# Performance work log

Hardware: AMD Instinct MI355X
Metric: run time of the kernel (lower is better)

## Reference

```python
import jax, jax.numpy as jnp
import numpy as np

THRE = 4.0  # ReLUX threshold / multispike lens
EPS = 1e-5  # BatchNorm eps (torch default)

@jax.custom_vjp
def spike(x):
    # multispike forward: floor(clamp(x,0,4)+0.5)
    return jnp.floor(jnp.clip(x, 0.0, THRE) + 0.5)

def _spike_fwd(x):
    return spike(x), x

def _spike_bwd(x, g):
    # surrogate gradient: pass-through on 0 < x < lens
    return (g * ((x > 0) & (x < THRE)).astype(g.dtype),)

spike.defvjp(_spike_fwd, _spike_bwd)


def setup_inputs() -> dict:
    key = jax.random.key(0)
    k0, k1, k2 = jax.random.split(key, 3)
    B, N, C = 4, 1024, 512
    x = jax.random.normal(k0, (B, N, C), jnp.float32)
    Wqkv = jax.random.normal(k1, (3 * C, C), jnp.float32) * (C ** -0.5)  # Linear weight [out,in], no bias
    gamma = jnp.ones((3 * C,), jnp.float32)   # BN weight
    beta = jnp.zeros((3 * C,), jnp.float32)   # BN bias
    Wproj = jax.random.normal(k2, (C, C), jnp.float32) * (C ** -0.5)
    bproj = jnp.zeros((C,), jnp.float32)
    return {"x": x, "Wqkv": Wqkv, "gamma": gamma, "beta": beta, "Wproj": Wproj, "bproj": bproj}


def reference(x, Wqkv, gamma, beta, Wproj, bproj):
    B, N, C = x.shape
    H = 8
    hd = C // H
    scale = hd ** -0.5

    xs = spike(x)                                    # head_spike
    qkv = jnp.einsum('bnc,dc->bnd', xs, Wqkv)        # [B,N,3C]
    # BatchNorm1d over channel dim with batch stats across (B, N)
    mu = qkv.mean(axis=(0, 1))
    var = qkv.var(axis=(0, 1))
    qkv = (qkv - mu) * jax.lax.rsqrt(var + EPS) * gamma + beta

    qkv = qkv.reshape(B, N, 3, H, hd).transpose(2, 0, 3, 1, 4)  # [3,B,H,N,hd]
    q = spike(qkv[0])
    k = spike(qkv[1])
    v = spike(qkv[2])

    attn = jnp.einsum('bhnd,bhmd->bhnm', q, k)       # no softmax
    attn = spike(attn)
    out = jnp.einsum('bhnm,bhmd->bhnd', attn, v) * scale
    out = out.transpose(0, 2, 1, 3).reshape(B, N, C)
    out = spike(out)                                 # project_spike
    return jnp.einsum('bnc,dc->bnd', out, Wproj) + bproj
```

## Files before the change

kernel.cpp:

```cpp
#include <hip/hip_runtime.h>

typedef __attribute__((ext_vector_type(8))) short short8;
typedef __attribute__((ext_vector_type(4))) short short4v;
typedef __attribute__((ext_vector_type(8))) signed char s8x8;
typedef __attribute__((ext_vector_type(4))) unsigned char u8x4;
typedef __attribute__((ext_vector_type(4))) float f32x4;
typedef __attribute__((ext_vector_type(4))) int int4v;
typedef __attribute__((ext_vector_type(4))) unsigned int u32x4;

#define THRE 4.0f

#define GLOAD_LDS16(g, l) \
    __builtin_amdgcn_global_load_lds((const __attribute__((address_space(1))) void*)(g), \
                                     (__attribute__((address_space(3))) void*)(l), 16, 0, 0)

__device__ __forceinline__ float spikef(float x) {
    return floorf(fminf(fmaxf(x, 0.0f), THRE) + 0.5f);
}
__device__ __forceinline__ unsigned short f2bf(float f) {
    return (unsigned short)(__builtin_bit_cast(unsigned int, f) >> 16);
}
__device__ __forceinline__ unsigned short f2bf_rn(float f) {
    unsigned u = __builtin_bit_cast(unsigned int, f);
    unsigned r = ((u >> 16) & 1u) + 0x7FFFu;
    return (unsigned short)((u + r) >> 16);
}
__device__ __forceinline__ float bf2f(unsigned short s) {
    return __builtin_bit_cast(float, (unsigned int)s << 16);
}
__device__ __forceinline__ int4v mfma_i8(u32x4 a, u32x4 b, int4v c) {
    return __builtin_amdgcn_mfma_i32_16x16x64_i8(__builtin_bit_cast(int4v, a),
                                                 __builtin_bit_cast(int4v, b), c, 0, 0, 0);
}

__global__ void k_prep(const float* __restrict__ x,
                       const float* __restrict__ Wq, const float* __restrict__ Wp,
                       unsigned char* __restrict__ xs8, signed char* __restrict__ Wq8,
                       float* __restrict__ wscale, short* __restrict__ Wpd) {
    const int blk = blockIdx.x, tid = threadIdx.x;
    if (blk < 2048) {
        const int i = blk * 256 + tid;
        const float4 v = *(const float4*)&x[(size_t)i * 4];
        u8x4 o;
        o.x = (unsigned char)spikef(v.x);
        o.y = (unsigned char)spikef(v.y);
        o.z = (unsigned char)spikef(v.z);
        o.w = (unsigned char)spikef(v.w);
        *(u8x4*)&xs8[(size_t)i * 4] = o;
    } else if (blk < 2432) {
        const int row = (blk - 2048) * 4 + (tid >> 6);
        const int lane = tid & 63;
        const float* wr = Wq + (size_t)row * 512 + lane * 8;
        float w[8];
        float mx = 0.f;
        #pragma unroll
        for (int i = 0; i < 8; ++i) { w[i] = wr[i]; mx = fmaxf(mx, fabsf(w[i])); }
        #pragma unroll
        for (int o = 32; o > 0; o >>= 1) mx = fmaxf(mx, __shfl_xor(mx, o, 64));
        const float inv = mx > 0.f ? 127.0f / mx : 0.f;
        s8x8 q;
        #pragma unroll
        for (int i = 0; i < 8; ++i) q[i] = (signed char)rintf(w[i] * inv);
        *(s8x8*)&Wq8[(size_t)row * 512 + lane * 8] = q;
        if (lane == 0) wscale[row] = mx > 0.f ? mx / 127.0f : 0.f;
    } else {
        const int i = (blk - 2432) * 256 + tid;
        const float4 v = *(const float4*)&Wp[(size_t)i * 4];
        short4v o;
        o.x = (short)f2bf_rn(v.x);
        o.y = (short)f2bf_rn(v.y);
        o.z = (short)f2bf_rn(v.z);
        o.w = (short)f2bf_rn(v.w);
        *(short4v*)&Wpd[(size_t)i * 4] = o;
    }
}

__global__ __launch_bounds__(256) void k_gemm_qkv(const unsigned char* __restrict__ A,
                                                  const signed char* __restrict__ B,
                                                  const float* __restrict__ wscale,
                                                  short* __restrict__ C,
                                                  float* __restrict__ psum,
                                                  float* __restrict__ psq) {
    __shared__ __align__(16) unsigned char As[128 * 128];
    __shared__ __align__(16) unsigned char Bs[96 * 128];
    const int tid  = threadIdx.x;
    const int lane = tid & 63, wv = tid >> 6;
    const int wy = wv >> 1, wx = wv & 1;
    const int quad = lane >> 4, l16 = lane & 15;
    const int u = blockIdx.x;
    const int mtile = u & 31;
    const int m0 = mtile * 128, n0 = (u >> 5) * 96;
    const int N = 1536;

    int4v acc[4][3];
    #pragma unroll
    for (int i = 0; i < 4; ++i)
        #pragma unroll
        for (int j = 0; j < 3; ++j)
            #pragma unroll
            for (int r = 0; r < 4; ++r) acc[i][j][r] = 0;

    const unsigned char* gA[4]; unsigned char* lA[4];
    #pragma unroll
    for (int i = 0; i < 4; ++i) {
        int L = wv + 4 * i;
        int c = L * 64 + lane;
        int r = c >> 3, g = (c & 7) ^ (r & 7);
        gA[i] = A + (size_t)(m0 + r) * 512 + g * 16;
        lA[i] = &As[(size_t)c * 16];
    }
    const unsigned char* gB[3]; unsigned char* lB[3];
    #pragma unroll
    for (int i = 0; i < 3; ++i) {
        int L = wv + 4 * i;
        int c = L * 64 + lane;
        int r = c >> 3, g = (c & 7) ^ (r & 7);
        gB[i] = (const unsigned char*)B + (size_t)(n0 + r) * 512 + g * 16;
        lB[i] = &Bs[(size_t)c * 16];
    }

    for (int k0 = 0; k0 < 512; k0 += 128) {
        __syncthreads();
        #pragma unroll
        for (int i = 0; i < 4; ++i) GLOAD_LDS16(gA[i] + k0, lA[i]);
        #pragma unroll
        for (int i = 0; i < 3; ++i) GLOAD_LDS16(gB[i] + k0, lB[i]);
        __syncthreads();
        #pragma unroll
        for (int kk = 0; kk < 2; ++kk) {
            u32x4 aF[4], bF[3];
            #pragma unroll
            for (int mt = 0; mt < 4; ++mt) {
                const int r = wy * 64 + mt * 16 + l16;
                aF[mt] = *(const u32x4*)&As[(size_t)r * 128 + (((kk * 4 + quad) ^ (r & 7)) * 16)];
            }
            #pragma unroll
            for (int nt = 0; nt < 3; ++nt) {
                const int r = wx * 48 + nt * 16 + l16;
                bF[nt] = *(const u32x4*)&Bs[(size_t)r * 128 + (((kk * 4 + quad) ^ (r & 7)) * 16)];
            }
            #pragma unroll
            for (int mt = 0; mt < 4; ++mt)
                #pragma unroll
                for (int nt = 0; nt < 3; ++nt)
                    acc[mt][nt] = mfma_i8(aF[mt], bF[nt], acc[mt][nt]);
        }
    }

    float sc[3];
    #pragma unroll
    for (int nt = 0; nt < 3; ++nt) sc[nt] = wscale[n0 + wx * 48 + nt * 16 + l16];

    float vacc[4][3][4];
    #pragma unroll
    for (int mt = 0; mt < 4; ++mt)
        #pragma unroll
        for (int r = 0; r < 4; ++r) {
            int row = m0 + wy * 64 + mt * 16 + quad * 4 + r;
            short* Cr = C + (size_t)row * N + n0 + wx * 48 + l16;
            #pragma unroll
            for (int nt = 0; nt < 3; ++nt) {
                float v = (float)acc[mt][nt][r] * sc[nt];
                vacc[mt][nt][r] = v;
                Cr[nt * 16] = (short)f2bf_rn(v);
            }
        }

    __syncthreads();
    float* PS = (float*)As;
    float* PQ = (float*)Bs;
    #pragma unroll
    for (int nt = 0; nt < 3; ++nt) {
        float s = 0.f, q = 0.f;
        #pragma unroll
        for (int mt = 0; mt < 4; ++mt)
            #pragma unroll
            for (int r = 0; r < 4; ++r) {
                float v = vacc[mt][nt][r];
                s += v;
                q = fmaf(v, v, q);
            }
        PS[(wy * 4 + quad) * 96 + wx * 48 + nt * 16 + l16] = s;
        PQ[(wy * 4 + quad) * 96 + wx * 48 + nt * 16 + l16] = q;
    }
    __syncthreads();
    if (tid < 96) {
        float s = 0.f, q = 0.f;
        #pragma unroll
        for (int i = 0; i < 8; ++i) { s += PS[i * 96 + tid]; q += PQ[i * 96 + tid]; }
        psum[mtile * 1536 + n0 + tid] = s;
        psq [mtile * 1536 + n0 + tid] = q;
    }
}

__global__ __launch_bounds__(256) void k_gemm_proj(const short* __restrict__ A,
                                                   const short* __restrict__ B,
                                                   const float* __restrict__ bias,
                                                   float* __restrict__ C) {
    __shared__ __align__(16) short As[32 * 64];
    __shared__ __align__(16) short Bs[128 * 64];
    const int tid  = threadIdx.x;
    const int lane = tid & 63, wv = tid >> 6;
    const int wy = wv >> 1, wx = wv & 1;
    const int quad = lane >> 4, l16 = lane & 15;
    const int u = blockIdx.x;
    const int mtile = u & 127;
    const int m0 = mtile * 32, n0 = (u >> 7) * 128;
    const int K = 512, N = 512;

    f32x4 acc[4];
    #pragma unroll
    for (int j = 0; j < 4; ++j)
        #pragma unroll
        for (int r = 0; r < 4; ++r) acc[j][r] = 0.f;

    const short* gA0; short* lA0;
    {
        int c = tid;
        int r = c >> 3, g = (c & 7) ^ (r & 7);
        gA0 = A + (size_t)(m0 + r) * K + g * 8;
        lA0 = &As[(size_t)c * 8];
    }
    const short* gB[4]; short* lB[4];
    #pragma unroll
    for (int i = 0; i < 4; ++i) {
        int c = tid + 256 * i;
        int r = c >> 3, g = (c & 7) ^ (r & 7);
        gB[i] = B + (size_t)(n0 + r) * K + g * 8;
        lB[i] = &Bs[(size_t)c * 8];
    }

    for (int k0 = 0; k0 < K; k0 += 64) {
        __syncthreads();
        GLOAD_LDS16(gA0 + k0, lA0);
        #pragma unroll
        for (int i = 0; i < 4; ++i) GLOAD_LDS16(gB[i] + k0, lB[i]);
        __syncthreads();
        #pragma unroll
        for (int kk = 0; kk < 2; ++kk) {
            const int ra = wy * 16 + l16;
            short8 aF = *(const short8*)&As[(size_t)ra * 64 + (((kk * 4 + quad) ^ (ra & 7)) * 8)];
            #pragma unroll
            for (int nt = 0; nt < 4; ++nt) {
                const int rb = wx * 64 + nt * 16 + l16;
                short8 bF = *(const short8*)&Bs[(size_t)rb * 64 + (((kk * 4 + quad) ^ (rb & 7)) * 8)];
                acc[nt] = __builtin_amdgcn_mfma_f32_16x16x32_bf16(aF, bF, acc[nt], 0, 0, 0);
            }
        }
    }

    float bs[4];
    #pragma unroll
    for (int nt = 0; nt < 4; ++nt) bs[nt] = bias[n0 + wx * 64 + nt * 16 + l16];
    #pragma unroll
    for (int r = 0; r < 4; ++r) {
        int row = m0 + wy * 16 + quad * 4 + r;
        float* Cr = C + (size_t)row * N + n0 + wx * 64 + l16;
        #pragma unroll
        for (int nt = 0; nt < 4; ++nt) Cr[nt * 16] = acc[nt][r] + bs[nt];
    }
}

__global__ __launch_bounds__(256) void k_bn_spike(const short* __restrict__ qkvb,
                           const float* __restrict__ psum, const float* __restrict__ psq,
                           const float* __restrict__ gamma, const float* __restrict__ beta,
                           unsigned char* __restrict__ qp, unsigned char* __restrict__ kp,
                           unsigned char* __restrict__ vt) {
    __shared__ float sa[64], sb[64];
    __shared__ __align__(16) unsigned char tile[64 * 80];
    const int tid = threadIdx.x;
    const int slice = blockIdx.x;
    const int c0 = slice * 64;
    const int r0 = blockIdx.y * 256;
    const int b = r0 >> 10, nb = r0 & 1023;

    if (tid < 64) {
        const int c = c0 + tid;
        double s = 0.0, q = 0.0;
        for (int st = 0; st < 32; ++st) { s += (double)psum[st * 1536 + c]; q += (double)psq[st * 1536 + c]; }
        const double mu  = s / 4096.0;
        const double var = q / 4096.0 - mu * mu;
        const float a = (float)((double)gamma[c] / sqrt(var + 1e-5));
        sa[tid] = a;
        sb[tid] = fmaf(-(float)mu, a, beta[c]);
    }
    __syncthreads();

    if (slice < 16) {
        const int h = slice & 7;
        const int ch4 = (tid & 15) * 4, rr = tid >> 4;
        const float4 A4 = *(const float4*)&sa[ch4];
        const float4 B4 = *(const float4*)&sb[ch4];
        unsigned char* base = (slice < 8 ? qp : kp) + (((size_t)b * 8 + h) * 1024 + nb) * 64;
        for (int i = rr; i < 256; i += 16) {
            const short4v v4 = *(const short4v*)&qkvb[(size_t)(r0 + i) * 1536 + c0 + ch4];
            u8x4 o;
            o.x = (unsigned char)spikef(fmaf(bf2f((unsigned short)v4.x), A4.x, B4.x));
            o.y = (unsigned char)spikef(fmaf(bf2f((unsigned short)v4.y), A4.y, B4.y));
            o.z = (unsigned char)spikef(fmaf(bf2f((unsigned short)v4.z), A4.z, B4.z));
            o.w = (unsigned char)spikef(fmaf(bf2f((unsigned short)v4.w), A4.w, B4.w));
            *(u8x4*)&base[(size_t)i * 64 + ch4] = o;
        }
    } else {
        const int h = slice - 16;
        const int ch = tid & 63, rq = tid >> 6;
        const float A = sa[ch], Bsh = sb[ch];
        const int e = tid >> 2, j0 = (tid & 3) * 16;
        unsigned char* vbase = vt + (size_t)b * 524288 + (size_t)h * 65536
                             + (size_t)(nb >> 8) * 16384 + e * 64 + j0;
        for (int rb = 0; rb < 4; ++rb) {
            __syncthreads();
            for (int i = rq; i < 64; i += 4) {
                float v = bf2f((unsigned short)qkvb[(size_t)(r0 + rb * 64 + i) * 1536 + c0 + ch]);
                tile[ch * 80 + i] = (unsigned char)spikef(fmaf(v, A, Bsh));
            }
            __syncthreads();
            *(u32x4*)&vbase[rb * 4096] = *(const u32x4*)&tile[e * 80 + j0];
        }
    }
}

__global__ __launch_bounds__(256) void k_attn(const unsigned char* __restrict__ qp,
                                              const unsigned char* __restrict__ kp,
                                              const unsigned char* __restrict__ vt,
                                              short* __restrict__ sout) {
    __shared__ __align__(16) unsigned int Sb[2][64 * 68];
    const int tid  = threadIdx.x;
    const int lane = tid & 63, w = tid >> 6;
    const int quad = lane >> 4, l16 = lane & 15;
    const int u = blockIdx.x;
    const int bhid = u & 31;
    const int b = bhid >> 3, h = bhid & 7;
    const int n0 = (u >> 5) * 64;
    const size_t bh = (size_t)b * 8 + h;

    const unsigned char* Kb = kp + bh * 65536;
    const unsigned char* Vb = vt + bh * 65536;

    u32x4 qf[4];
    #pragma unroll
    for (int mt = 0; mt < 4; ++mt)
        qf[mt] = *(const u32x4*)&qp[(bh * 1024 + n0 + mt * 16 + l16) * 64 + quad * 16];

    int4v of[4];
    #pragma unroll
    for (int mt = 0; mt < 4; ++mt)
        #pragma unroll
        for (int r = 0; r < 4; ++r) of[mt][r] = 0;

    u32x4 kfc[4];
    #pragma unroll
    for (int jt = 0; jt < 4; ++jt)
        kfc[jt] = *(const u32x4*)&Kb[(size_t)(w * 64 + jt * 16 + l16) * 64 + quad * 16];

    #pragma unroll
    for (int t = 0; t < 4; ++t) {
        u32x4 bV[4];
        #pragma unroll
        for (int kk = 0; kk < 4; ++kk)
            bV[kk] = *(const u32x4*)&Vb[(size_t)((t * 4 + kk) * 64 + w * 16 + l16) * 64 + quad * 16];

        __builtin_amdgcn_s_setprio(1);
        #pragma unroll
        for (int jt = 0; jt < 4; ++jt) {
            #pragma unroll
            for (int mt = 0; mt < 4; ++mt) {
                int4v z;
                #pragma unroll
                for (int r = 0; r < 4; ++r) z[r] = 0;
                int4v s = mfma_i8(kfc[jt], qf[mt], z);
                unsigned int pkk = 0;
                #pragma unroll
                for (int r = 0; r < 4; ++r) {
                    int v = s[r]; v = v < 0 ? 0 : (v > 4 ? 4 : v);
                    pkk |= (unsigned int)v << (8 * r);
                }
                Sb[t & 1][(mt * 16 + l16) * 68 + w * 16 + jt * 4 + quad] = pkk;
            }
        }
        __builtin_amdgcn_s_setprio(0);
        __syncthreads();

        if (t < 3) {
            #pragma unroll
            for (int jt = 0; jt < 4; ++jt)
                kfc[jt] = *(const u32x4*)&Kb[(size_t)((t + 1) * 256 + w * 64 + jt * 16 + l16) * 64 + quad * 16];
        }

        __builtin_amdgcn_s_setprio(1);
        #pragma unroll
        for (int kk = 0; kk < 4; ++kk) {
            #pragma unroll
            for (int mt = 0; mt < 4; ++mt) {
                u32x4 aS = *(const u32x4*)&Sb[t & 1][(mt * 16 + l16) * 68 + kk * 16 + quad * 4];
                of[mt] = mfma_i8(aS, bV[kk], of[mt]);
            }
        }
        __builtin_amdgcn_s_setprio(0);
    }

    #pragma unroll
    for (int mt = 0; mt < 4; ++mt)
        #pragma unroll
        for (int r = 0; r < 4; ++r) {
            size_t orow = (size_t)b * 1024 + n0 + mt * 16 + quad * 4 + r;
            sout[orow * 512 + h * 64 + w * 16 + l16] =
                (short)f2bf(spikef((float)of[mt][r] * 0.125f));
        }
}

extern "C" void kernel_launch(void* const* d_in, const int* in_sizes, int n_in,
                              void* d_out, int out_size, void* d_ws, size_t ws_size,
                              hipStream_t stream) {
    const float* x     = (const float*)d_in[0];
    const float* Wqkv  = (const float*)d_in[1];
    const float* gamma = (const float*)d_in[2];
    const float* beta  = (const float*)d_in[3];
    const float* Wproj = (const float*)d_in[4];
    const float* bproj = (const float*)d_in[5];
    float* out = (float*)d_out;

    char* w = (char*)d_ws;
    unsigned char* xs8   = (unsigned char*)(w);
    signed char* Wq8     = (signed char*)(w + 8388608);
    float* wscale        = (float*)(w + 9437184);
    short* Wproj2        = (short*)(w + 11534336);
    short* qkvb          = (short*)(w + 12582912);
    unsigned char* qp    = (unsigned char*)(w + 37748736);
    unsigned char* kp    = (unsigned char*)(w + 41943040);
    unsigned char* vt    = (unsigned char*)(w + 46137344);
    float* psum          = (float*)(w + 50331648);
    float* psq           = psum + 32 * 1536;
    short* sout          = (short*)(w);

    k_prep<<<2688, 256, 0, stream>>>(x, Wqkv, Wproj, xs8, Wq8, wscale, Wproj2);
    k_gemm_qkv<<<512, 256, 0, stream>>>(xs8, Wq8, wscale, qkvb, psum, psq);
    k_bn_spike<<<dim3(24, 16), 256, 0, stream>>>(qkvb, psum, psq, gamma, beta, qp, kp, vt);
    k_attn<<<512, 256, 0, stream>>>(qp, kp, vt, sout);
    k_gemm_proj<<<512, 256, 0, stream>>>(sout, Wproj2, bproj, out);
}
```

Before: 108.9 us.

## Fuse input spike and weight int8 quantization into QKV GEMM, drop prep kernel

```diff
diff --git a/kernel.cpp b/kernel.cpp
--- a/kernel.cpp
+++ b/kernel.cpp
@@ -2,7 +2,6 @@
 
 typedef __attribute__((ext_vector_type(8))) short short8;
 typedef __attribute__((ext_vector_type(4))) short short4v;
-typedef __attribute__((ext_vector_type(8))) signed char s8x8;
 typedef __attribute__((ext_vector_type(4))) unsigned char u8x4;
 typedef __attribute__((ext_vector_type(4))) float f32x4;
 typedef __attribute__((ext_vector_type(4))) int int4v;
@@ -33,56 +32,14 @@
                                                  __builtin_bit_cast(int4v, b), c, 0, 0, 0);
 }
 
-__global__ void k_prep(const float* __restrict__ x,
-                       const float* __restrict__ Wq, const float* __restrict__ Wp,
-                       unsigned char* __restrict__ xs8, signed char* __restrict__ Wq8,
-                       float* __restrict__ wscale, short* __restrict__ Wpd) {
-    const int blk = blockIdx.x, tid = threadIdx.x;
-    if (blk < 2048) {
-        const int i = blk * 256 + tid;
-        const float4 v = *(const float4*)&x[(size_t)i * 4];
-        u8x4 o;
-        o.x = (unsigned char)spikef(v.x);
-        o.y = (unsigned char)spikef(v.y);
-        o.z = (unsigned char)spikef(v.z);
-        o.w = (unsigned char)spikef(v.w);
-        *(u8x4*)&xs8[(size_t)i * 4] = o;
-    } else if (blk < 2432) {
-        const int row = (blk - 2048) * 4 + (tid >> 6);
-        const int lane = tid & 63;
-        const float* wr = Wq + (size_t)row * 512 + lane * 8;
-        float w[8];
-        float mx = 0.f;
-        #pragma unroll
-        for (int i = 0; i < 8; ++i) { w[i] = wr[i]; mx = fmaxf(mx, fabsf(w[i])); }
-        #pragma unroll
-        for (int o = 32; o > 0; o >>= 1) mx = fmaxf(mx, __shfl_xor(mx, o, 64));
-        const float inv = mx > 0.f ? 127.0f / mx : 0.f;
-        s8x8 q;
-        #pragma unroll
-        for (int i = 0; i < 8; ++i) q[i] = (signed char)rintf(w[i] * inv);
-        *(s8x8*)&Wq8[(size_t)row * 512 + lane * 8] = q;
-        if (lane == 0) wscale[row] = mx > 0.f ? mx / 127.0f : 0.f;
-    } else {
-        const int i = (blk - 2432) * 256 + tid;
-        const float4 v = *(const float4*)&Wp[(size_t)i * 4];
-        short4v o;
-        o.x = (short)f2bf_rn(v.x);
-        o.y = (short)f2bf_rn(v.y);
-        o.z = (short)f2bf_rn(v.z);
-        o.w = (short)f2bf_rn(v.w);
-        *(short4v*)&Wpd[(size_t)i * 4] = o;
-    }
-}
-
-__global__ __launch_bounds__(256) void k_gemm_qkv(const unsigned char* __restrict__ A,
-                                                  const signed char* __restrict__ B,
-                                                  const float* __restrict__ wscale,
-                                                  short* __restrict__ C,
-                                                  float* __restrict__ psum,
-                                                  float* __restrict__ psq) {
+__global__ __launch_bounds__(256, 2) void k_qkv(const float* __restrict__ x,
+                                                const float* __restrict__ Wq,
+                                                short* __restrict__ C,
+                                                float* __restrict__ psum,
+                                                float* __restrict__ psq) {
     __shared__ __align__(16) unsigned char As[128 * 128];
-    __shared__ __align__(16) unsigned char Bs[96 * 128];
+    __shared__ __align__(16) unsigned char Bs[96 * 512];
+    __shared__ float invB[96], scB[96];
     const int tid  = threadIdx.x;
     const int lane = tid & 63, wv = tid >> 6;
     const int wy = wv >> 1, wx = wv & 1;
@@ -92,6 +49,56 @@
     const int m0 = mtile * 128, n0 = (u >> 5) * 96;
     const int N = 1536;
 
+    #pragma unroll
+    for (int rr = 0; rr < 3; ++rr) {
+        const int row = rr * 32 + (tid >> 3);
+        const int ln8 = tid & 7;
+        const float* wr = Wq + (size_t)(n0 + row) * 512 + ln8 * 64;
+        float mx = 0.f;
+        #pragma unroll
+        for (int i = 0; i < 16; ++i) {
+            const float4 f = *(const float4*)(wr + i * 4);
+            mx = fmaxf(mx, fmaxf(fmaxf(fabsf(f.x), fabsf(f.y)), fmaxf(fabsf(f.z), fabsf(f.w))));
+        }
+        mx = fmaxf(mx, __shfl_xor(mx, 1, 64));
+        mx = fmaxf(mx, __shfl_xor(mx, 2, 64));
+        mx = fmaxf(mx, __shfl_xor(mx, 4, 64));
+        if (ln8 == 0) {
+            invB[row] = mx > 0.f ? 127.0f / mx : 0.f;
+            scB[row]  = mx > 0.f ? mx / 127.0f : 0.f;
+        }
+    }
+    __syncthreads();
+
+    #pragma unroll
+    for (int i = 0; i < 12; ++i) {
+        const int idx = i * 256 + tid;
+        const int r = idx >> 5, ks = idx & 31;
+        const float* src = Wq + (size_t)(n0 + r) * 512 + ks * 16;
+        const float inv = invB[r];
+        u32x4 ov;
+        #pragma unroll
+        for (int d = 0; d < 4; ++d) {
+            const float4 f = *(const float4*)(src + d * 4);
+            unsigned dw  = ((unsigned)(int)rintf(f.x * inv)) & 255u;
+            dw |= (((unsigned)(int)rintf(f.y * inv)) & 255u) << 8;
+            dw |= (((unsigned)(int)rintf(f.z * inv)) & 255u) << 16;
+            dw |= (((unsigned)(int)rintf(f.w * inv)) & 255u) << 24;
+            ov[d] = dw;
+        }
+        *(u32x4*)&Bs[(size_t)r * 512 + (((ks & ~7) | ((ks & 7) ^ (r & 7))) * 16)] = ov;
+    }
+
+    float4 aPre[16];
+    #pragma unroll
+    for (int i = 0; i < 4; ++i) {
+        const int idx = i * 256 + tid;
+        const int r = idx >> 3, q = idx & 7;
+        const float* src = x + (size_t)(m0 + r) * 512 + q * 16;
+        #pragma unroll
+        for (int d = 0; d < 4; ++d) aPre[i * 4 + d] = *(const float4*)(src + d * 4);
+    }
+
     int4v acc[4][3];
     #pragma unroll
     for (int i = 0; i < 4; ++i)
@@ -100,32 +107,37 @@
             #pragma unroll
             for (int r = 0; r < 4; ++r) acc[i][j][r] = 0;
 
-    const unsigned char* gA[4]; unsigned char* lA[4];
-    #pragma unroll
-    for (int i = 0; i < 4; ++i) {
-        int L = wv + 4 * i;
-        int c = L * 64 + lane;
-        int r = c >> 3, g = (c & 7) ^ (r & 7);
-        gA[i] = A + (size_t)(m0 + r) * 512 + g * 16;
-        lA[i] = &As[(size_t)c * 16];
-    }
-    const unsigned char* gB[3]; unsigned char* lB[3];
-    #pragma unroll
-    for (int i = 0; i < 3; ++i) {
-        int L = wv + 4 * i;
-        int c = L * 64 + lane;
-        int r = c >> 3, g = (c & 7) ^ (r & 7);
-        gB[i] = (const unsigned char*)B + (size_t)(n0 + r) * 512 + g * 16;
-        lB[i] = &Bs[(size_t)c * 16];
-    }
-
-    for (int k0 = 0; k0 < 512; k0 += 128) {
+    for (int t = 0; t < 4; ++t) {
         __syncthreads();
         #pragma unroll
-        for (int i = 0; i < 4; ++i) GLOAD_LDS16(gA[i] + k0, lA[i]);
-        #pragma unroll
-        for (int i = 0; i < 3; ++i) GLOAD_LDS16(gB[i] + k0, lB[i]);
+        for (int i = 0; i < 4; ++i) {
+            const int idx = i * 256 + tid;
+            const int r = idx >> 3, q = idx & 7;
+            u32x4 ov;
+            #pragma unroll
+            for (int d = 0; d < 4; ++d) {
+                const float4 f = aPre[i * 4 + d];
+                unsigned dw  = (unsigned)(unsigned char)spikef(f.x);
+                dw |= (unsigned)(unsigned char)spikef(f.y) << 8;
+                dw |= (unsigned)(unsigned char)spikef(f.z) << 16;
+                dw |= (unsigned)(unsigned char)spikef(f.w) << 24;
+                ov[d] = dw;
+            }
+            *(u32x4*)&As[(size_t)r * 128 + ((q ^ (r & 7)) * 16)] = ov;
+        }
         __syncthreads();
+        if (t < 3) {
+            const int k0n = (t + 1) * 128;
+            #pragma unroll
+            for (int i = 0; i < 4; ++i) {
+                const int idx = i * 256 + tid;
+                const int r = idx >> 3, q = idx & 7;
+                const float* src = x + (size_t)(m0 + r) * 512 + k0n + q * 16;
+                #pragma unroll
+                for (int d = 0; d < 4; ++d) aPre[i * 4 + d] = *(const float4*)(src + d * 4);
+            }
+        }
+        const int k0 = t * 128;
         #pragma unroll
         for (int kk = 0; kk < 2; ++kk) {
             u32x4 aF[4], bF[3];
@@ -137,7 +149,7 @@
             #pragma unroll
             for (int nt = 0; nt < 3; ++nt) {
                 const int r = wx * 48 + nt * 16 + l16;
-                bF[nt] = *(const u32x4*)&Bs[(size_t)r * 128 + (((kk * 4 + quad) ^ (r & 7)) * 16)];
+                bF[nt] = *(const u32x4*)&Bs[(size_t)r * 512 + k0 + (((kk * 4 + quad) ^ (r & 7)) * 16)];
             }
             #pragma unroll
             for (int mt = 0; mt < 4; ++mt)
@@ -149,7 +161,7 @@
 
     float sc[3];
     #pragma unroll
-    for (int nt = 0; nt < 3; ++nt) sc[nt] = wscale[n0 + wx * 48 + nt * 16 + l16];
+    for (int nt = 0; nt < 3; ++nt) sc[nt] = scB[wx * 48 + nt * 16 + l16];
 
     float vacc[4][3][4];
     #pragma unroll
@@ -191,6 +203,168 @@
         psum[mtile * 1536 + n0 + tid] = s;
         psq [mtile * 1536 + n0 + tid] = q;
     }
+}
+
+__global__ __launch_bounds__(256) void k_bn_spike(const short* __restrict__ qkvb,
+                           const float* __restrict__ psum, const float* __restrict__ psq,
+                           const float* __restrict__ gamma, const float* __restrict__ beta,
+                           unsigned char* __restrict__ qp, unsigned char* __restrict__ kp,
+                           unsigned char* __restrict__ vt,
+                           const float* __restrict__ Wp, short* __restrict__ Wpd) {
+    __shared__ float sa[64], sb[64];
+    __shared__ __align__(16) unsigned char tile[64 * 80];
+    const int tid = threadIdx.x;
+    const int slice = blockIdx.x;
+    const int c0 = slice * 64;
+    const int r0 = blockIdx.y * 256;
+    const int b = r0 >> 10, nb = r0 & 1023;
+
+    {
+        const int gid = (blockIdx.y * 24 + blockIdx.x) * 256 + tid;
+        if (gid < 65536) {
+            const float4 v = *(const float4*)&Wp[(size_t)gid * 4];
+            short4v o;
+            o.x = (short)f2bf_rn(v.x);
+            o.y = (short)f2bf_rn(v.y);
+            o.z = (short)f2bf_rn(v.z);
+            o.w = (short)f2bf_rn(v.w);
+            *(short4v*)&Wpd[(size_t)gid * 4] = o;
+        }
+    }
+
+    if (tid < 64) {
+        const int c = c0 + tid;
+        double s = 0.0, q = 0.0;
+        for (int st = 0; st < 32; ++st) { s += (double)psum[st * 1536 + c]; q += (double)psq[st * 1536 + c]; }
+        const double mu  = s / 4096.0;
+        const double var = q / 4096.0 - mu * mu;
+        const float a = (float)((double)gamma[c] / sqrt(var + 1e-5));
+        sa[tid] = a;
+        sb[tid] = fmaf(-(float)mu, a, beta[c]);
+    }
+    __syncthreads();
+
+    if (slice < 16) {
+        const int h = slice & 7;
+        const int ch4 = (tid & 15) * 4, rr = tid >> 4;
+        const float4 A4 = *(const float4*)&sa[ch4];
+        const float4 B4 = *(const float4*)&sb[ch4];
+        unsigned char* base = (slice < 8 ? qp : kp) + (((size_t)b * 8 + h) * 1024 + nb) * 64;
+        for (int i = rr; i < 256; i += 16) {
+            const short4v v4 = *(const short4v*)&qkvb[(size_t)(r0 + i) * 1536 + c0 + ch4];
+            u8x4 o;
+            o.x = (unsigned char)spikef(fmaf(bf2f((unsigned short)v4.x), A4.x, B4.x));
+            o.y = (unsigned char)spikef(fmaf(bf2f((unsigned short)v4.y), A4.y, B4.y));
+            o.z = (unsigned char)spikef(fmaf(bf2f((unsigned short)v4.z), A4.z, B4.z));
+            o.w = (unsigned char)spikef(fmaf(bf2f((unsigned short)v4.w), A4.w, B4.w));
+            *(u8x4*)&base[(size_t)i * 64 + ch4] = o;
+        }
+    } else {
+        const int h = slice - 16;
+        const int ch = tid & 63, rq = tid >> 6;
+        const float A = sa[ch], Bsh = sb[ch];
+        const int e = tid >> 2, j0 = (tid & 3) * 16;
+        unsigned char* vbase = vt + (size_t)b * 524288 + (size_t)h * 65536
+                             + (size_t)(nb >> 8) * 16384 + e * 64 + j0;
+        for (int rb = 0; rb < 4; ++rb) {
+            __syncthreads();
+            for (int i = rq; i < 64; i += 4) {
+                float v = bf2f((unsigned short)qkvb[(size_t)(r0 + rb * 64 + i) * 1536 + c0 + ch]);
+                tile[ch * 80 + i] = (unsigned char)spikef(fmaf(v, A, Bsh));
+            }
+            __syncthreads();
+            *(u32x4*)&vbase[rb * 4096] = *(const u32x4*)&tile[e * 80 + j0];
+        }
+    }
+}
+
+__global__ __launch_bounds__(256) void k_attn(const unsigned char* __restrict__ qp,
+                                              const unsigned char* __restrict__ kp,
+                                              const unsigned char* __restrict__ vt,
+                                              short* __restrict__ sout) {
+    __shared__ __align__(16) unsigned int Sb[2][64 * 68];
+    const int tid  = threadIdx.x;
+    const int lane = tid & 63, w = tid >> 6;
+    const int quad = lane >> 4, l16 = lane & 15;
+    const int u = blockIdx.x;
+    const int bhid = u & 31;
+    const int b = bhid >> 3, h = bhid & 7;
+    const int n0 = (u >> 5) * 64;
+    const size_t bh = (size_t)b * 8 + h;
+
+    const unsigned char* Kb = kp + bh * 65536;
+    const unsigned char* Vb = vt + bh * 65536;
+
+    u32x4 qf[4];
+    #pragma unroll
+    for (int mt = 0; mt < 4; ++mt)
+        qf[mt] = *(const u32x4*)&qp[(bh * 1024 + n0 + mt * 16 + l16) * 64 + quad * 16];
+
+    int4v of[4];
+    #pragma unroll
+    for (int mt = 0; mt < 4; ++mt)
+        #pragma unroll
+        for (int r = 0; r < 4; ++r) of[mt][r] = 0;
+
+    u32x4 kfc[4];
+    #pragma unroll
+    for (int jt = 0; jt < 4; ++jt)
+        kfc[jt] = *(const u32x4*)&Kb[(size_t)(w * 64 + jt * 16 + l16) * 64 + quad * 16];
+
+    #pragma unroll
+    for (int t = 0; t < 4; ++t) {
+        u32x4 bV[4];
+        #pragma unroll
+        for (int kk = 0; kk < 4; ++kk)
+            bV[kk] = *(const u32x4*)&Vb[(size_t)((t * 4 + kk) * 64 + w * 16 + l16) * 64 + quad * 16];
+
+        __builtin_amdgcn_s_setprio(1);
+        #pragma unroll
+        for (int jt = 0; jt < 4; ++jt) {
+            #pragma unroll
+            for (int mt = 0; mt < 4; ++mt) {
+                int4v z;
+                #pragma unroll
+                for (int r = 0; r < 4; ++r) z[r] = 0;
+                int4v s = mfma_i8(kfc[jt], qf[mt], z);
+                unsigned int pkk = 0;
+                #pragma unroll
+                for (int r = 0; r < 4; ++r) {
+                    int v = s[r]; v = v < 0 ? 0 : (v > 4 ? 4 : v);
+                    pkk |= (unsigned int)v << (8 * r);
+                }
+                Sb[t & 1][(mt * 16 + l16) * 68 + w * 16 + jt * 4 + quad] = pkk;
+            }
+        }
+        __builtin_amdgcn_s_setprio(0);
+        __syncthreads();
+
+        if (t < 3) {
+            #pragma unroll
+            for (int jt = 0; jt < 4; ++jt)
+                kfc[jt] = *(const u32x4*)&Kb[(size_t)((t + 1) * 256 + w * 64 + jt * 16 + l16) * 64 + quad * 16];
+        }
+
+        __builtin_amdgcn_s_setprio(1);
+        #pragma unroll
+        for (int kk = 0; kk < 4; ++kk) {
+            #pragma unroll
+            for (int mt = 0; mt < 4; ++mt) {
+                u32x4 aS = *(const u32x4*)&Sb[t & 1][(mt * 16 + l16) * 68 + kk * 16 + quad * 4];
+                of[mt] = mfma_i8(aS, bV[kk], of[mt]);
+            }
+        }
+        __builtin_amdgcn_s_setprio(0);
+    }
+
+    #pragma unroll
+    for (int mt = 0; mt < 4; ++mt)
+        #pragma unroll
+        for (int r = 0; r < 4; ++r) {
+            size_t orow = (size_t)b * 1024 + n0 + mt * 16 + quad * 4 + r;
+            sout[orow * 512 + h * 64 + w * 16 + l16] =
+                (short)f2bf(spikef((float)of[mt][r] * 0.125f));
+        }
 }
 
 __global__ __launch_bounds__(256) void k_gemm_proj(const short* __restrict__ A,
@@ -261,154 +435,6 @@
     }
 }
 
-__global__ __launch_bounds__(256) void k_bn_spike(const short* __restrict__ qkvb,
-                           const float* __restrict__ psum, const float* __restrict__ psq,
-                           const float* __restrict__ gamma, const float* __restrict__ beta,
-                           unsigned char* __restrict__ qp, unsigned char* __restrict__ kp,
-                           unsigned char* __restrict__ vt) {
-    __shared__ float sa[64], sb[64];
-    __shared__ __align__(16) unsigned char tile[64 * 80];
-    const int tid = threadIdx.x;
-    const int slice = blockIdx.x;
-    const int c0 = slice * 64;
-    const int r0 = blockIdx.y * 256;
-    const int b = r0 >> 10, nb = r0 & 1023;
-
-    if (tid < 64) {
-        const int c = c0 + tid;
-        double s = 0.0, q = 0.0;
-        for (int st = 0; st < 32; ++st) { s += (double)psum[st * 1536 + c]; q += (double)psq[st * 1536 + c]; }
-        const double mu  = s / 4096.0;
-        const double var = q / 4096.0 - mu * mu;
-        const float a = (float)((double)gamma[c] / sqrt(var + 1e-5));
-        sa[tid] = a;
-        sb[tid] = fmaf(-(float)mu, a, beta[c]);
-    }
-    __syncthreads();
-
-    if (slice < 16) {
-        const int h = slice & 7;
-        const int ch4 = (tid & 15) * 4, rr = tid >> 4;
-        const float4 A4 = *(const float4*)&sa[ch4];
-        const float4 B4 = *(const float4*)&sb[ch4];
-        unsigned char* base = (slice < 8 ? qp : kp) + (((size_t)b * 8 + h) * 1024 + nb) * 64;
-        for (int i = rr; i < 256; i += 16) {
-            const short4v v4 = *(const short4v*)&qkvb[(size_t)(r0 + i) * 1536 + c0 + ch4];
-            u8x4 o;
-            o.x = (unsigned char)spikef(fmaf(bf2f((unsigned short)v4.x), A4.x, B4.x));
-            o.y = (unsigned char)spikef(fmaf(bf2f((unsigned short)v4.y), A4.y, B4.y));
-            o.z = (unsigned char)spikef(fmaf(bf2f((unsigned short)v4.z), A4.z, B4.z));
-            o.w = (unsigned char)spikef(fmaf(bf2f((unsigned short)v4.w), A4.w, B4.w));
-            *(u8x4*)&base[(size_t)i * 64 + ch4] = o;
-        }
-    } else {
-        const int h = slice - 16;
-        const int ch = tid & 63, rq = tid >> 6;
-        const float A = sa[ch], Bsh = sb[ch];
-        const int e = tid >> 2, j0 = (tid & 3) * 16;
-        unsigned char* vbase = vt + (size_t)b * 524288 + (size_t)h * 65536
-                             + (size_t)(nb >> 8) * 16384 + e * 64 + j0;
-        for (int rb = 0; rb < 4; ++rb) {
-            __syncthreads();
-            for (int i = rq; i < 64; i += 4) {
-                float v = bf2f((unsigned short)qkvb[(size_t)(r0 + rb * 64 + i) * 1536 + c0 + ch]);
-                tile[ch * 80 + i] = (unsigned char)spikef(fmaf(v, A, Bsh));
-            }
-            __syncthreads();
-            *(u32x4*)&vbase[rb * 4096] = *(const u32x4*)&tile[e * 80 + j0];
-        }
-    }
-}
-
-__global__ __launch_bounds__(256) void k_attn(const unsigned char* __restrict__ qp,
-                                              const unsigned char* __restrict__ kp,
-                                              const unsigned char* __restrict__ vt,
-                                              short* __restrict__ sout) {
-    __shared__ __align__(16) unsigned int Sb[2][64 * 68];
-    const int tid  = threadIdx.x;
-    const int lane = tid & 63, w = tid >> 6;
-    const int quad = lane >> 4, l16 = lane & 15;
-    const int u = blockIdx.x;
-    const int bhid = u & 31;
-    const int b = bhid >> 3, h = bhid & 7;
-    const int n0 = (u >> 5) * 64;
-    const size_t bh = (size_t)b * 8 + h;
-
-    const unsigned char* Kb = kp + bh * 65536;
-    const unsigned char* Vb = vt + bh * 65536;
-
-    u32x4 qf[4];
-    #pragma unroll
-    for (int mt = 0; mt < 4; ++mt)
-        qf[mt] = *(const u32x4*)&qp[(bh * 1024 + n0 + mt * 16 + l16) * 64 + quad * 16];
-
-    int4v of[4];
-    #pragma unroll
-    for (int mt = 0; mt < 4; ++mt)
-        #pragma unroll
-        for (int r = 0; r < 4; ++r) of[mt][r] = 0;
-
-    u32x4 kfc[4];
-    #pragma unroll
-    for (int jt = 0; jt < 4; ++jt)
-        kfc[jt] = *(const u32x4*)&Kb[(size_t)(w * 64 + jt * 16 + l16) * 64 + quad * 16];
-
-    #pragma unroll
-    for (int t = 0; t < 4; ++t) {
-        u32x4 bV[4];
-        #pragma unroll
-        for (int kk = 0; kk < 4; ++kk)
-            bV[kk] = *(const u32x4*)&Vb[(size_t)((t * 4 + kk) * 64 + w * 16 + l16) * 64 + quad * 16];
-
-        __builtin_amdgcn_s_setprio(1);
-        #pragma unroll
-        for (int jt = 0; jt < 4; ++jt) {
-            #pragma unroll
-            for (int mt = 0; mt < 4; ++mt) {
-                int4v z;
-                #pragma unroll
-                for (int r = 0; r < 4; ++r) z[r] = 0;
-                int4v s = mfma_i8(kfc[jt], qf[mt], z);
-                unsigned int pkk = 0;
-                #pragma unroll
-                for (int r = 0; r < 4; ++r) {
-                    int v = s[r]; v = v < 0 ? 0 : (v > 4 ? 4 : v);
-                    pkk |= (unsigned int)v << (8 * r);
-                }
-                Sb[t & 1][(mt * 16 + l16) * 68 + w * 16 + jt * 4 + quad] = pkk;
-            }
-        }
-        __builtin_amdgcn_s_setprio(0);
-        __syncthreads();
-
-        if (t < 3) {
-            #pragma unroll
-            for (int jt = 0; jt < 4; ++jt)
-                kfc[jt] = *(const u32x4*)&Kb[(size_t)((t + 1) * 256 + w * 64 + jt * 16 + l16) * 64 + quad * 16];
-        }
-
-        __builtin_amdgcn_s_setprio(1);
-        #pragma unroll
-        for (int kk = 0; kk < 4; ++kk) {
-            #pragma unroll
-            for (int mt = 0; mt < 4; ++mt) {
-                u32x4 aS = *(const u32x4*)&Sb[t & 1][(mt * 16 + l16) * 68 + kk * 16 + quad * 4];
-                of[mt] = mfma_i8(aS, bV[kk], of[mt]);
-            }
-        }
-        __builtin_amdgcn_s_setprio(0);
-    }
-
-    #pragma unroll
-    for (int mt = 0; mt < 4; ++mt)
-        #pragma unroll
-        for (int r = 0; r < 4; ++r) {
-            size_t orow = (size_t)b * 1024 + n0 + mt * 16 + quad * 4 + r;
-            sout[orow * 512 + h * 64 + w * 16 + l16] =
-                (short)f2bf(spikef((float)of[mt][r] * 0.125f));
-        }
-}
-
 extern "C" void kernel_launch(void* const* d_in, const int* in_sizes, int n_in,
                               void* d_out, int out_size, void* d_ws, size_t ws_size,
                               hipStream_t stream) {
@@ -421,10 +447,7 @@
     float* out = (float*)d_out;
 
     char* w = (char*)d_ws;
-    unsigned char* xs8   = (unsigned char*)(w);
-    signed char* Wq8     = (signed char*)(w + 8388608);
-    float* wscale        = (float*)(w + 9437184);
-    short* Wproj2        = (short*)(w + 11534336);
+    short* Wpd           = (short*)(w + 11534336);
     short* qkvb          = (short*)(w + 12582912);
     unsigned char* qp    = (unsigned char*)(w + 37748736);
     unsigned char* kp    = (unsigned char*)(w + 41943040);
@@ -433,9 +456,8 @@
     float* psq           = psum + 32 * 1536;
     short* sout          = (short*)(w);
 
-    k_prep<<<2688, 256, 0, stream>>>(x, Wqkv, Wproj, xs8, Wq8, wscale, Wproj2);
-    k_gemm_qkv<<<512, 256, 0, stream>>>(xs8, Wq8, wscale, qkvb, psum, psq);
-    k_bn_spike<<<dim3(24, 16), 256, 0, stream>>>(qkvb, psum, psq, gamma, beta, qp, kp, vt);
-    k_attn<<<512, 256, 0, stream>>>(qp, kp, vt, sout);
-    k_gemm_proj<<<512, 256, 0, stream>>>(sout, Wproj2, bproj, out);
-}
+    k_qkv      <<<512, 256, 0, stream>>>(x, Wqkv, qkvb, psum, psq);
+    k_bn_spike <<<dim3(24, 16), 256, 0, stream>>>(qkvb, psum, psq, gamma, beta, qp, kp, vt, Wproj, Wpd);
+    k_attn     <<<512, 256, 0, stream>>>(qp, kp, vt, sout);
+    k_gemm_proj<<<512, 256, 0, stream>>>(sout, Wpd, bproj, out);
+}
```

Result: slower. 126.7 us (+16.3%).

## Double-buffer GEMM LDS loads, move Wproj cast into BN kernel, widen BN loads

Applied to the files above, without the earlier changes.

```diff
diff --git a/kernel.cpp b/kernel.cpp
--- a/kernel.cpp
+++ b/kernel.cpp
@@ -13,6 +13,10 @@
 #define GLOAD_LDS16(g, l) \
     __builtin_amdgcn_global_load_lds((const __attribute__((address_space(1))) void*)(g), \
                                      (__attribute__((address_space(3))) void*)(l), 16, 0, 0)
+#define WAIT_VM(n)  asm volatile("s_waitcnt vmcnt(" #n ")" ::: "memory")
+#define WAIT_LGKM0  asm volatile("s_waitcnt lgkmcnt(0)" ::: "memory")
+#define SBAR        __builtin_amdgcn_s_barrier()
+#define SCHEDBAR    __builtin_amdgcn_sched_barrier(0)
 
 __device__ __forceinline__ float spikef(float x) {
     return floorf(fminf(fmaxf(x, 0.0f), THRE) + 0.5f);
@@ -33,10 +37,9 @@
                                                  __builtin_bit_cast(int4v, b), c, 0, 0, 0);
 }
 
-__global__ void k_prep(const float* __restrict__ x,
-                       const float* __restrict__ Wq, const float* __restrict__ Wp,
+__global__ void k_prep(const float* __restrict__ x, const float* __restrict__ Wq,
                        unsigned char* __restrict__ xs8, signed char* __restrict__ Wq8,
-                       float* __restrict__ wscale, short* __restrict__ Wpd) {
+                       float* __restrict__ wscale) {
     const int blk = blockIdx.x, tid = threadIdx.x;
     if (blk < 2048) {
         const int i = blk * 256 + tid;
@@ -47,7 +50,7 @@
         o.z = (unsigned char)spikef(v.z);
         o.w = (unsigned char)spikef(v.w);
         *(u8x4*)&xs8[(size_t)i * 4] = o;
-    } else if (blk < 2432) {
+    } else {
         const int row = (blk - 2048) * 4 + (tid >> 6);
         const int lane = tid & 63;
         const float* wr = Wq + (size_t)row * 512 + lane * 8;
@@ -63,15 +66,6 @@
         for (int i = 0; i < 8; ++i) q[i] = (signed char)rintf(w[i] * inv);
         *(s8x8*)&Wq8[(size_t)row * 512 + lane * 8] = q;
         if (lane == 0) wscale[row] = mx > 0.f ? mx / 127.0f : 0.f;
-    } else {
-        const int i = (blk - 2432) * 256 + tid;
-        const float4 v = *(const float4*)&Wp[(size_t)i * 4];
-        short4v o;
-        o.x = (short)f2bf_rn(v.x);
-        o.y = (short)f2bf_rn(v.y);
-        o.z = (short)f2bf_rn(v.z);
-        o.w = (short)f2bf_rn(v.w);
-        *(short4v*)&Wpd[(size_t)i * 4] = o;
     }
 }
 
@@ -81,8 +75,8 @@
                                                   short* __restrict__ C,
                                                   float* __restrict__ psum,
                                                   float* __restrict__ psq) {
-    __shared__ __align__(16) unsigned char As[128 * 128];
-    __shared__ __align__(16) unsigned char Bs[96 * 128];
+    __shared__ __align__(16) unsigned char As[2][128 * 128];
+    __shared__ __align__(16) unsigned char Bs[2][96 * 128];
     const int tid  = threadIdx.x;
     const int lane = tid & 63, wv = tid >> 6;
     const int wy = wv >> 1, wx = wv & 1;
@@ -92,6 +86,11 @@
     const int m0 = mtile * 128, n0 = (u >> 5) * 96;
     const int N = 1536;
 
+    float sc[3];
+    #pragma unroll
+    for (int nt = 0; nt < 3; ++nt) sc[nt] = wscale[n0 + wx * 48 + nt * 16 + l16];
+    asm volatile("" :: "v"(sc[0]), "v"(sc[1]), "v"(sc[2]));
+
     int4v acc[4][3];
     #pragma unroll
     for (int i = 0; i < 4; ++i)
@@ -100,44 +99,59 @@
             #pragma unroll
             for (int r = 0; r < 4; ++r) acc[i][j][r] = 0;
 
-    const unsigned char* gA[4]; unsigned char* lA[4];
+    const unsigned char* gA[4]; int lA[4];
     #pragma unroll
     for (int i = 0; i < 4; ++i) {
-        int L = wv + 4 * i;
-        int c = L * 64 + lane;
+        int c = (wv + 4 * i) * 64 + lane;
         int r = c >> 3, g = (c & 7) ^ (r & 7);
         gA[i] = A + (size_t)(m0 + r) * 512 + g * 16;
-        lA[i] = &As[(size_t)c * 16];
-    }
-    const unsigned char* gB[3]; unsigned char* lB[3];
+        lA[i] = c * 16;
+    }
+    const unsigned char* gB[3]; int lB[3];
     #pragma unroll
     for (int i = 0; i < 3; ++i) {
-        int L = wv + 4 * i;
-        int c = L * 64 + lane;
+        int c = (wv + 4 * i) * 64 + lane;
         int r = c >> 3, g = (c & 7) ^ (r & 7);
         gB[i] = (const unsigned char*)B + (size_t)(n0 + r) * 512 + g * 16;
-        lB[i] = &Bs[(size_t)c * 16];
-    }
-
-    for (int k0 = 0; k0 < 512; k0 += 128) {
-        __syncthreads();
-        #pragma unroll
-        for (int i = 0; i < 4; ++i) GLOAD_LDS16(gA[i] + k0, lA[i]);
-        #pragma unroll
-        for (int i = 0; i < 3; ++i) GLOAD_LDS16(gB[i] + k0, lB[i]);
-        __syncthreads();
+        lB[i] = c * 16;
+    }
+
+    #pragma unroll
+    for (int i = 0; i < 4; ++i) GLOAD_LDS16(gA[i], &As[0][lA[i]]);
+    #pragma unroll
+    for (int i = 0; i < 3; ++i) GLOAD_LDS16(gB[i], &Bs[0][lB[i]]);
+
+    for (int t = 0; t < 4; ++t) {
+        if (t > 0) {
+            WAIT_LGKM0;
+            SBAR;
+        }
+        if (t < 3) {
+            const int k0n = (t + 1) * 128;
+            const int bn = (t + 1) & 1;
+            #pragma unroll
+            for (int i = 0; i < 4; ++i) GLOAD_LDS16(gA[i] + k0n, &As[bn][lA[i]]);
+            #pragma unroll
+            for (int i = 0; i < 3; ++i) GLOAD_LDS16(gB[i] + k0n, &Bs[bn][lB[i]]);
+            WAIT_VM(7);
+        } else {
+            WAIT_VM(0);
+        }
+        SBAR;
+        SCHEDBAR;
+        const int bc = t & 1;
         #pragma unroll
         for (int kk = 0; kk < 2; ++kk) {
             u32x4 aF[4], bF[3];
             #pragma unroll
             for (int mt = 0; mt < 4; ++mt) {
                 const int r = wy * 64 + mt * 16 + l16;
-                aF[mt] = *(const u32x4*)&As[(size_t)r * 128 + (((kk * 4 + quad) ^ (r & 7)) * 16)];
+                aF[mt] = *(const u32x4*)&As[bc][(size_t)r * 128 + (((kk * 4 + quad) ^ (r & 7)) * 16)];
             }
             #pragma unroll
             for (int nt = 0; nt < 3; ++nt) {
                 const int r = wx * 48 + nt * 16 + l16;
-                bF[nt] = *(const u32x4*)&Bs[(size_t)r * 128 + (((kk * 4 + quad) ^ (r & 7)) * 16)];
+                bF[nt] = *(const u32x4*)&Bs[bc][(size_t)r * 128 + (((kk * 4 + quad) ^ (r & 7)) * 16)];
             }
             #pragma unroll
             for (int mt = 0; mt < 4; ++mt)
@@ -147,10 +161,6 @@
         }
     }
 
-    float sc[3];
-    #pragma unroll
-    for (int nt = 0; nt < 3; ++nt) sc[nt] = wscale[n0 + wx * 48 + nt * 16 + l16];
-
     float vacc[4][3][4];
     #pragma unroll
     for (int mt = 0; mt < 4; ++mt)
@@ -167,8 +177,8 @@
         }
 
     __syncthreads();
-    float* PS = (float*)As;
-    float* PQ = (float*)Bs;
+    float* PS = (float*)&As[0][0];
+    float* PQ = (float*)&As[1][0];
     #pragma unroll
     for (int nt = 0; nt < 3; ++nt) {
         float s = 0.f, q = 0.f;
@@ -193,79 +203,12 @@
     }
 }
 
-__global__ __launch_bounds__(256) void k_gemm_proj(const short* __restrict__ A,
-                                                   const short* __restrict__ B,
-                                                   const float* __restrict__ bias,
-                                                   float* __restrict__ C) {
-    __shared__ __align__(16) short As[32 * 64];
-    __shared__ __align__(16) short Bs[128 * 64];
-    const int tid  = threadIdx.x;
-    const int lane = tid & 63, wv = tid >> 6;
-    const int wy = wv >> 1, wx = wv & 1;
-    const int quad = lane >> 4, l16 = lane & 15;
-    const int u = blockIdx.x;
-    const int mtile = u & 127;
-    const int m0 = mtile * 32, n0 = (u >> 7) * 128;
-    const int K = 512, N = 512;
-
-    f32x4 acc[4];
-    #pragma unroll
-    for (int j = 0; j < 4; ++j)
-        #pragma unroll
-        for (int r = 0; r < 4; ++r) acc[j][r] = 0.f;
-
-    const short* gA0; short* lA0;
-    {
-        int c = tid;
-        int r = c >> 3, g = (c & 7) ^ (r & 7);
-        gA0 = A + (size_t)(m0 + r) * K + g * 8;
-        lA0 = &As[(size_t)c * 8];
-    }
-    const short* gB[4]; short* lB[4];
-    #pragma unroll
-    for (int i = 0; i < 4; ++i) {
-        int c = tid + 256 * i;
-        int r = c >> 3, g = (c & 7) ^ (r & 7);
-        gB[i] = B + (size_t)(n0 + r) * K + g * 8;
-        lB[i] = &Bs[(size_t)c * 8];
-    }
-
-    for (int k0 = 0; k0 < K; k0 += 64) {
-        __syncthreads();
-        GLOAD_LDS16(gA0 + k0, lA0);
-        #pragma unroll
-        for (int i = 0; i < 4; ++i) GLOAD_LDS16(gB[i] + k0, lB[i]);
-        __syncthreads();
-        #pragma unroll
-        for (int kk = 0; kk < 2; ++kk) {
-            const int ra = wy * 16 + l16;
-            short8 aF = *(const short8*)&As[(size_t)ra * 64 + (((kk * 4 + quad) ^ (ra & 7)) * 8)];
-            #pragma unroll
-            for (int nt = 0; nt < 4; ++nt) {
-                const int rb = wx * 64 + nt * 16 + l16;
-                short8 bF = *(const short8*)&Bs[(size_t)rb * 64 + (((kk * 4 + quad) ^ (rb & 7)) * 8)];
-                acc[nt] = __builtin_amdgcn_mfma_f32_16x16x32_bf16(aF, bF, acc[nt], 0, 0, 0);
-            }
-        }
-    }
-
-    float bs[4];
-    #pragma unroll
-    for (int nt = 0; nt < 4; ++nt) bs[nt] = bias[n0 + wx * 64 + nt * 16 + l16];
-    #pragma unroll
-    for (int r = 0; r < 4; ++r) {
-        int row = m0 + wy * 16 + quad * 4 + r;
-        float* Cr = C + (size_t)row * N + n0 + wx * 64 + l16;
-        #pragma unroll
-        for (int nt = 0; nt < 4; ++nt) Cr[nt * 16] = acc[nt][r] + bs[nt];
-    }
-}
-
 __global__ __launch_bounds__(256) void k_bn_spike(const short* __restrict__ qkvb,
                            const float* __restrict__ psum, const float* __restrict__ psq,
                            const float* __restrict__ gamma, const float* __restrict__ beta,
                            unsigned char* __restrict__ qp, unsigned char* __restrict__ kp,
-                           unsigned char* __restrict__ vt) {
+                           unsigned char* __restrict__ vt,
+                           const float* __restrict__ Wp, short* __restrict__ Wpd) {
     __shared__ float sa[64], sb[64];
     __shared__ __align__(16) unsigned char tile[64 * 80];
     const int tid = threadIdx.x;
@@ -273,6 +216,19 @@
     const int c0 = slice * 64;
     const int r0 = blockIdx.y * 256;
     const int b = r0 >> 10, nb = r0 & 1023;
+
+    {
+        const int gid = (blockIdx.y * 24 + blockIdx.x) * 256 + tid;
+        if (gid < 65536) {
+            const float4 v = *(const float4*)&Wp[(size_t)gid * 4];
+            short4v o;
+            o.x = (short)f2bf_rn(v.x);
+            o.y = (short)f2bf_rn(v.y);
+            o.z = (short)f2bf_rn(v.z);
+            o.w = (short)f2bf_rn(v.w);
+            *(short4v*)&Wpd[(size_t)gid * 4] = o;
+        }
+    }
 
     if (tid < 64) {
         const int c = c0 + tid;
@@ -286,33 +242,43 @@
     }
     __syncthreads();
 
+    const int ch8 = (tid & 7) * 8;
+    float A8[8], B8[8];
+    #pragma unroll
+    for (int j = 0; j < 8; ++j) { A8[j] = sa[ch8 + j]; B8[j] = sb[ch8 + j]; }
+
     if (slice < 16) {
         const int h = slice & 7;
-        const int ch4 = (tid & 15) * 4, rr = tid >> 4;
-        const float4 A4 = *(const float4*)&sa[ch4];
-        const float4 B4 = *(const float4*)&sb[ch4];
+        const int rr = tid >> 3;
         unsigned char* base = (slice < 8 ? qp : kp) + (((size_t)b * 8 + h) * 1024 + nb) * 64;
-        for (int i = rr; i < 256; i += 16) {
-            const short4v v4 = *(const short4v*)&qkvb[(size_t)(r0 + i) * 1536 + c0 + ch4];
-            u8x4 o;
-            o.x = (unsigned char)spikef(fmaf(bf2f((unsigned short)v4.x), A4.x, B4.x));
-            o.y = (unsigned char)spikef(fmaf(bf2f((unsigned short)v4.y), A4.y, B4.y));
-            o.z = (unsigned char)spikef(fmaf(bf2f((unsigned short)v4.z), A4.z, B4.z));
-            o.w = (unsigned char)spikef(fmaf(bf2f((unsigned short)v4.w), A4.w, B4.w));
-            *(u8x4*)&base[(size_t)i * 64 + ch4] = o;
+        for (int i = rr; i < 256; i += 32) {
+            const short8 v8 = *(const short8*)&qkvb[(size_t)(r0 + i) * 1536 + c0 + ch8];
+            unsigned lo = 0, hi = 0;
+            #pragma unroll
+            for (int j = 0; j < 4; ++j)
+                lo |= (unsigned)(unsigned char)spikef(fmaf(bf2f((unsigned short)v8[j]), A8[j], B8[j])) << (8 * j);
+            #pragma unroll
+            for (int j = 0; j < 4; ++j)
+                hi |= (unsigned)(unsigned char)spikef(fmaf(bf2f((unsigned short)v8[4 + j]), A8[4 + j], B8[4 + j])) << (8 * j);
+            uint2 o; o.x = lo; o.y = hi;
+            *(uint2*)&base[(size_t)i * 64 + ch8] = o;
         }
     } else {
         const int h = slice - 16;
-        const int ch = tid & 63, rq = tid >> 6;
-        const float A = sa[ch], Bsh = sb[ch];
+        const int rw = tid >> 3;
         const int e = tid >> 2, j0 = (tid & 3) * 16;
         unsigned char* vbase = vt + (size_t)b * 524288 + (size_t)h * 65536
                              + (size_t)(nb >> 8) * 16384 + e * 64 + j0;
         for (int rb = 0; rb < 4; ++rb) {
             __syncthreads();
-            for (int i = rq; i < 64; i += 4) {
-                float v = bf2f((unsigned short)qkvb[(size_t)(r0 + rb * 64 + i) * 1536 + c0 + ch]);
-                tile[ch * 80 + i] = (unsigned char)spikef(fmaf(v, A, Bsh));
+            #pragma unroll
+            for (int p = 0; p < 2; ++p) {
+                const int row = p * 32 + rw;
+                const short8 v8 = *(const short8*)&qkvb[(size_t)(r0 + rb * 64 + row) * 1536 + c0 + ch8];
+                #pragma unroll
+                for (int j = 0; j < 8; ++j)
+                    tile[(ch8 + j) * 80 + row] =
+                        (unsigned char)spikef(fmaf(bf2f((unsigned short)v8[j]), A8[j], B8[j]));
             }
             __syncthreads();
             *(u32x4*)&vbase[rb * 4096] = *(const u32x4*)&tile[e * 80 + j0];
@@ -409,6 +375,92 @@
         }
 }
 
+__global__ __launch_bounds__(256) void k_gemm_proj(const short* __restrict__ A,
+                                                   const short* __restrict__ B,
+                                                   const float* __restrict__ bias,
+                                                   float* __restrict__ C) {
+    __shared__ __align__(16) short As[32 * 512];
+    __shared__ __align__(16) short Bs[2][128 * 64];
+    const int tid  = threadIdx.x;
+    const int lane = tid & 63, wv = tid >> 6;
+    const int wy = wv >> 1, wx = wv & 1;
+    const int quad = lane >> 4, l16 = lane & 15;
+    const int u = blockIdx.x;
+    const int mtile = u & 127;
+    const int m0 = mtile * 32, n0 = (u >> 7) * 128;
+    const int N = 512;
+
+    float bs[4];
+    #pragma unroll
+    for (int nt = 0; nt < 4; ++nt) bs[nt] = bias[n0 + wx * 64 + nt * 16 + l16];
+    asm volatile("" :: "v"(bs[0]), "v"(bs[1]), "v"(bs[2]), "v"(bs[3]));
+
+    f32x4 acc[4];
+    #pragma unroll
+    for (int j = 0; j < 4; ++j)
+        #pragma unroll
+        for (int r = 0; r < 4; ++r) acc[j][r] = 0.f;
+
+    const short* gAg[8]; int lAo[8];
+    #pragma unroll
+    for (int i = 0; i < 8; ++i) {
+        int c = tid + 256 * i;
+        int r = c >> 6, slot = c & 63, kb = slot >> 3, s8 = slot & 7;
+        gAg[i] = A + (size_t)(m0 + r) * 512 + (kb * 8 + (s8 ^ (r & 7))) * 8;
+        lAo[i] = c * 8;
+    }
+    const short* gBg[4]; int lBo[4];
+    #pragma unroll
+    for (int i = 0; i < 4; ++i) {
+        int c = tid + 256 * i;
+        int r = c >> 3, s8 = c & 7;
+        gBg[i] = B + (size_t)(n0 + r) * 512 + (s8 ^ (r & 7)) * 8;
+        lBo[i] = c * 8;
+    }
+
+    #pragma unroll
+    for (int i = 0; i < 8; ++i) GLOAD_LDS16(gAg[i], &As[lAo[i]]);
+    #pragma unroll
+    for (int i = 0; i < 4; ++i) GLOAD_LDS16(gBg[i], &Bs[0][lBo[i]]);
+
+    for (int t = 0; t < 8; ++t) {
+        if (t > 0) {
+            WAIT_LGKM0;
+            SBAR;
+        }
+        if (t < 7) {
+            const int bn = (t + 1) & 1;
+            #pragma unroll
+            for (int i = 0; i < 4; ++i) GLOAD_LDS16(gBg[i] + (t + 1) * 64, &Bs[bn][lBo[i]]);
+            WAIT_VM(4);
+        } else {
+            WAIT_VM(0);
+        }
+        SBAR;
+        SCHEDBAR;
+        const int bc = t & 1;
+        #pragma unroll
+        for (int kk = 0; kk < 2; ++kk) {
+            const int ra = wy * 16 + l16;
+            short8 aF = *(const short8*)&As[(size_t)ra * 512 + t * 64 + (((kk * 4 + quad) ^ (ra & 7)) * 8)];
+            #pragma unroll
+            for (int nt = 0; nt < 4; ++nt) {
+                const int rb = wx * 64 + nt * 16 + l16;
+                short8 bF = *(const short8*)&Bs[bc][(size_t)rb * 64 + (((kk * 4 + quad) ^ (rb & 7)) * 8)];
+                acc[nt] = __builtin_amdgcn_mfma_f32_16x16x32_bf16(aF, bF, acc[nt], 0, 0, 0);
+            }
+        }
+    }
+
+    #pragma unroll
+    for (int r = 0; r < 4; ++r) {
+        int row = m0 + wy * 16 + quad * 4 + r;
+        float* Cr = C + (size_t)row * N + n0 + wx * 64 + l16;
+        #pragma unroll
+        for (int nt = 0; nt < 4; ++nt) Cr[nt * 16] = acc[nt][r] + bs[nt];
+    }
+}
+
 extern "C" void kernel_launch(void* const* d_in, const int* in_sizes, int n_in,
                               void* d_out, int out_size, void* d_ws, size_t ws_size,
                               hipStream_t stream) {
@@ -424,7 +476,7 @@
     unsigned char* xs8   = (unsigned char*)(w);
     signed char* Wq8     = (signed char*)(w + 8388608);
     float* wscale        = (float*)(w + 9437184);
-    short* Wproj2        = (short*)(w + 11534336);
+    short* Wpd           = (short*)(w + 11534336);
     short* qkvb          = (short*)(w + 12582912);
     unsigned char* qp    = (unsigned char*)(w + 37748736);
     unsigned char* kp    = (unsigned char*)(w + 41943040);
@@ -433,9 +485,9 @@
     float* psq           = psum + 32 * 1536;
     short* sout          = (short*)(w);
 
-    k_prep<<<2688, 256, 0, stream>>>(x, Wqkv, Wproj, xs8, Wq8, wscale, Wproj2);
-    k_gemm_qkv<<<512, 256, 0, stream>>>(xs8, Wq8, wscale, qkvb, psum, psq);
-    k_bn_spike<<<dim3(24, 16), 256, 0, stream>>>(qkvb, psum, psq, gamma, beta, qp, kp, vt);
-    k_attn<<<512, 256, 0, stream>>>(qp, kp, vt, sout);
-    k_gemm_proj<<<512, 256, 0, stream>>>(sout, Wproj2, bproj, out);
-}
+    k_prep     <<<2432, 256, 0, stream>>>(x, Wqkv, xs8, Wq8, wscale);
+    k_gemm_qkv <<<512, 256, 0, stream>>>(xs8, Wq8, wscale, qkvb, psum, psq);
+    k_bn_spike <<<dim3(24, 16), 256, 0, stream>>>(qkvb, psum, psq, gamma, beta, qp, kp, vt, Wproj, Wpd);
+    k_attn     <<<512, 256, 0, stream>>>(qp, kp, vt, sout);
+    k_gemm_proj<<<512, 256, 0, stream>>>(sout, Wpd, bproj, out);
+}
```

After: 103.8 us. -4.7%, faster.
